# Optimization experiments

Hardware: AMD Instinct MI355X
Metric: run time of the kernel (lower is better)

The kernel has to match this reference:

```python
import jax, jax.numpy as jnp
from jax import lax
import numpy as np

B, CTX, TGT, D_MODEL = 2, 1024, 256, 512
EXPAND, D_STATE, D_CONV, N_LAYERS = 2, 16, 4, 2
D_INNER = EXPAND * D_MODEL
DT_RANK = (D_MODEL + 15) // 16  # 32, mamba_ssm default ceil(d_model/16)
LN_EPS = 1e-5


def setup_inputs() -> dict:
    key = jax.random.key(0)
    ks = jax.random.split(key, 20)
    s = 0.02
    inp = {
        "context_repr": jax.random.normal(ks[0], (B, CTX, D_MODEL), jnp.float32),
        "target_time_emb": jax.random.normal(ks[1], (B, TGT, D_MODEL), jnp.float32),
        "target_var_emb": jax.random.normal(ks[2], (B, TGT, D_MODEL), jnp.float32),
        "target_count": TGT,
        # position_proj / output_proj / LayerNorm params
        "pos_w": jax.random.normal(ks[3], (D_MODEL, 2 * D_MODEL), jnp.float32) * s,
        "pos_b": jnp.zeros((D_MODEL,), jnp.float32),
        "outp_w": jax.random.normal(ks[4], (D_MODEL, D_MODEL), jnp.float32) * s,
        "outp_b": jnp.zeros((D_MODEL,), jnp.float32),
        "ln_g": jnp.ones((D_MODEL,), jnp.float32),
        "ln_b": jnp.zeros((D_MODEL,), jnp.float32),
        # stacked per-layer Mamba params
        "in_w": jax.random.normal(ks[5], (N_LAYERS, 2 * D_INNER, D_MODEL), jnp.float32) * s,
        "conv_w": jax.random.normal(ks[6], (N_LAYERS, D_INNER, D_CONV), jnp.float32) * s,
        "conv_b": jnp.zeros((N_LAYERS, D_INNER), jnp.float32),
        "xproj_w": jax.random.normal(ks[7], (N_LAYERS, DT_RANK + 2 * D_STATE, D_INNER), jnp.float32) * s,
        "dt_w": jax.random.normal(ks[8], (N_LAYERS, D_INNER, DT_RANK), jnp.float32) * s,
        "dt_b": jax.random.normal(ks[9], (N_LAYERS, D_INNER), jnp.float32) * s,
        # A_log init as in mamba_ssm: A = arange(1, d_state+1) repeated over d_inner
        "A_log": jnp.broadcast_to(
            jnp.log(jnp.arange(1, D_STATE + 1, dtype=jnp.float32)),
            (N_LAYERS, D_INNER, D_STATE),
        ).copy(),
        "D_skip": jnp.ones((N_LAYERS, D_INNER), jnp.float32),
        "out_w": jax.random.normal(ks[10], (N_LAYERS, D_MODEL, D_INNER), jnp.float32) * s,
    }
    return inp


def _mamba_block(x, in_w, conv_w, conv_b, xproj_w, dt_w, dt_b, A_log, D_skip, out_w):
    # x: [B, L, d_model]
    Bb, L, _ = x.shape
    xz = jnp.einsum("bld,ed->ble", x, in_w)          # [B, L, 2*d_inner]
    xc, z = jnp.split(xz, 2, axis=-1)
    # causal depthwise conv1d (Conv1d pad=d_conv-1 then [..., :L])
    xt = xc.transpose(0, 2, 1)                        # [B, d_inner, L]
    conv = lax.conv_general_dilated(
        xt, conv_w[:, None, :], (1,), [(D_CONV - 1, 0)],
        feature_group_count=D_INNER,
        dimension_numbers=("NCH", "OIH", "NCH"),
    )
    u = jax.nn.silu(conv + conv_b[None, :, None]).transpose(0, 2, 1)  # [B, L, d_inner]
    x_dbl = jnp.einsum("bld,ed->ble", u, xproj_w)     # [B, L, dt_rank + 2*d_state]
    dt, Bm, Cm = jnp.split(x_dbl, [DT_RANK, DT_RANK + D_STATE], axis=-1)
    delta = jax.nn.softplus(jnp.einsum("blr,dr->bld", dt, dt_w) + dt_b)  # [B, L, d_inner]
    A = -jnp.exp(A_log)                               # [d_inner, d_state]
    dA = jnp.exp(delta[..., None] * A)                # [B, L, d_inner, d_state]
    dBu = delta[..., None] * Bm[:, :, None, :] * u[..., None]

    def step(h, inps):
        dA_t, dBu_t, C_t = inps                       # [B,d_inner,d_state], same, [B,d_state]
        h = dA_t * h + dBu_t
        y = jnp.einsum("bds,bs->bd", h, C_t)
        return h, y

    h0 = jnp.zeros((Bb, D_INNER, D_STATE), x.dtype)
    _, ys = lax.scan(step, h0, (dA.transpose(1, 0, 2, 3), dBu.transpose(1, 0, 2, 3), Cm.transpose(1, 0, 2)))
    y = ys.transpose(1, 0, 2) + u * D_skip            # [B, L, d_inner]
    y = y * jax.nn.silu(z)
    return jnp.einsum("ble,de->bld", y, out_w)        # [B, L, d_model]


def reference(context_repr, target_time_emb, target_var_emb, target_count,
              pos_w, pos_b, outp_w, outp_b, ln_g, ln_b,
              in_w, conv_w, conv_b, xproj_w, dt_w, dt_b, A_log, D_skip, out_w):
    tc = jnp.concatenate([target_time_emb, target_var_emb], axis=-1)      # [B, T, 2*d]
    pos = jnp.einsum("blk,dk->bld", tc, pos_w) + pos_b                    # [B, T, d]
    x = jnp.concatenate([context_repr, pos], axis=1)                      # [B, C+T, d]
    for i in range(N_LAYERS):
        x = x + _mamba_block(x, in_w[i], conv_w[i], conv_b[i], xproj_w[i],
                             dt_w[i], dt_b[i], A_log[i], D_skip[i], out_w[i])
    mu = jnp.mean(x, axis=-1, keepdims=True)
    var = jnp.mean(jnp.square(x - mu), axis=-1, keepdims=True)
    x = (x - mu) * lax.rsqrt(var + LN_EPS) * ln_g + ln_b
    tgt = x[:, -int(target_count):]
    return jnp.einsum("bld,ed->ble", tgt, outp_w) + outp_b
```

## Files before the change

### kernel.cpp

```cpp
#include <hip/hip_runtime.h>
#include <hip/hip_bf16.h>

#define B_     2
#define CTX_   1024
#define TGT_   256
#define DM_    512
#define L_     1280
#define DI_    1024
#define DS_    16
#define DCONV_ 4
#define NL_    2
#define DTR_   32
#define MROWS_ (B_*L_)
#define NC_    80
#define CL_    16
#define XDBL_N_ (MROWS_*64)

typedef unsigned short u16;
typedef __attribute__((ext_vector_type(8))) __bf16 bf16x8;
typedef __attribute__((ext_vector_type(4))) float f32x4;

__device__ __forceinline__ float sigmoidf_(float v){ return 1.f/(1.f+__expf(-v)); }
__device__ __forceinline__ float siluf_(float v){ return v*sigmoidf_(v); }
__device__ __forceinline__ float softplusf_(float v){ return (v>20.f)?v:log1pf(__expf(v)); }
__device__ __forceinline__ u16 f2b(float f){
    union { float f; unsigned u; } x; x.f = f;
    unsigned u = x.u;
    return (u16)((u + 0x7fffu + ((u>>16)&1u)) >> 16);
}
__device__ __forceinline__ float b2f(u16 v){ return __uint_as_float(((unsigned)v)<<16); }
__device__ __forceinline__ void gload_lds16(const void* g, void* l){
    __builtin_amdgcn_global_load_lds((const __attribute__((address_space(1))) unsigned*)g,
                                     (__attribute__((address_space(3))) unsigned*)l, 16, 0, 0);
}
#define PIPE_SYNC do{ asm volatile("s_waitcnt vmcnt(0)" ::: "memory"); \
                      __builtin_amdgcn_sched_barrier(0); \
                      __builtin_amdgcn_s_barrier(); \
                      __builtin_amdgcn_sched_barrier(0); }while(0)

#define G0_ 262144
#define G1_ 131072
#define G2_  65536
#define G3_  32768
#define G4_  16384
__global__ __launch_bounds__(256) void k_init(const float* __restrict__ s0, const float* __restrict__ s1,
                                              const float* __restrict__ s2, const float* __restrict__ s3,
                                              const float* __restrict__ s4,
                                              u16* d0, u16* d1, u16* d2, u16* d3, u16* d4,
                                              const float* __restrict__ ctx, const float* __restrict__ te,
                                              const float* __restrict__ ve, float* __restrict__ x,
                                              u16* __restrict__ xb, u16* __restrict__ tcb){
    int blk = blockIdx.x;
    if (blk < 1984){
        int g = blk*256 + threadIdx.x;
        const float* s; u16* d; int base;
        if      (g < G0_)                { s=s0; d=d0; base=g*8; }
        else if (g < G0_+G1_)            { s=s1; d=d1; base=(g-G0_)*8; }
        else if (g < G0_+G1_+G2_)        { s=s2; d=d2; base=(g-G0_-G1_)*8; }
        else if (g < G0_+G1_+G2_+G3_)    { s=s3; d=d3; base=(g-G0_-G1_-G2_)*8; }
        else                             { s=s4; d=d4; base=(g-G0_-G1_-G2_-G3_)*8; }
        float4 a = *(const float4*)&s[base];
        float4 b = *(const float4*)&s[base+4];
        union { u16 us[8]; uint4 v; } o;
        o.us[0]=f2b(a.x); o.us[1]=f2b(a.y); o.us[2]=f2b(a.z); o.us[3]=f2b(a.w);
        o.us[4]=f2b(b.x); o.us[5]=f2b(b.y); o.us[6]=f2b(b.z); o.us[7]=f2b(b.w);
        *(uint4*)&d[base] = o.v;
    } else if (blk < 1984+1024){
        int e = ((blk-1984)*256 + threadIdx.x)*4;
        int d = e % DM_;
        int l = (e/DM_) % CTX_;
        int b = e/(DM_*CTX_);
        float4 v = *(const float4*)&ctx[e];
        size_t o = ((size_t)(b*L_+l))*DM_ + d;
        *(float4*)&x[o] = v;
        union { u16 us[4]; uint2 q; } p;
        p.us[0]=f2b(v.x); p.us[1]=f2b(v.y); p.us[2]=f2b(v.z); p.us[3]=f2b(v.w);
        *(uint2*)&xb[o] = p.q;
    } else {
        int e = ((blk-1984-1024)*256 + threadIdx.x)*4;
        int k = e % (2*DM_);
        int r = e / (2*DM_);
        float4 v = (k < DM_) ? *(const float4*)&te[(size_t)r*DM_ + k]
                             : *(const float4*)&ve[(size_t)r*DM_ + (k-DM_)];
        union { u16 us[4]; uint2 q; } p;
        p.us[0]=f2b(v.x); p.us[1]=f2b(v.y); p.us[2]=f2b(v.z); p.us[3]=f2b(v.w);
        *(uint2*)&tcb[e] = p.q;
    }
}

template<bool WB>
__global__ __launch_bounds__(512) void k_mmx(const u16* __restrict__ A, int lda,
                                             const u16* __restrict__ Bw, int ldb,
                                             float* __restrict__ C, int ldc,
                                             const float* __restrict__ bias, int K,
                                             u16* __restrict__ Cb, int ldcb){
    __shared__ u16 As[2][128*64];
    __shared__ u16 Bs[2][128*64];
    int tid = threadIdx.x;
    int wave = tid >> 6, lane = tid & 63;
    int bm = blockIdx.y*128, bn = blockIdx.x*128;
    int wr = (wave>>2)*64, wc = (wave&3)*32;
    f32x4 acc[4][2] = {};
    int lrow = lane & 15, lk = (lane>>4)*8;
    int dphys0 = tid*16;
    int dphys1 = dphys0 + 8192;
    int alog0  = dphys0 ^ (((dphys0>>7)&7)<<4);
    int alog1  = dphys1 ^ (((dphys1>>7)&7)<<4);
    int grow0  = alog0 >> 7,         grow1 = alog1 >> 7;
    int gcol0  = (alog0 & 127) >> 1, gcol1 = (alog1 & 127) >> 1;
    const u16* Ar0 = A  + (size_t)(bm+grow0)*lda + gcol0;
    const u16* Ar1 = A  + (size_t)(bm+grow1)*lda + gcol1;
    const u16* Br0 = Bw + (size_t)(bn+grow0)*ldb + gcol0;
    const u16* Br1 = Bw + (size_t)(bn+grow1)*ldb + gcol1;
    int aoff[4][2], boff[2][2];
    #pragma unroll
    for (int f=0; f<4; ++f){
        int ra = wr + f*16 + lrow;
        #pragma unroll
        for (int s=0;s<2;++s) aoff[f][s] = (ra*128 + s*64 + lk*2) ^ ((ra&7)<<4);
    }
    #pragma unroll
    for (int f=0; f<2; ++f){
        int rb = wc + f*16 + lrow;
        #pragma unroll
        for (int s=0;s<2;++s) boff[f][s] = (rb*128 + s*64 + lk*2) ^ ((rb&7)<<4);
    }
    int nt = K >> 6;
    auto stage = [&](int t, int buf){
        int k0 = t*64;
        gload_lds16(Ar0 + k0, &As[buf][wave*512]);
        gload_lds16(Ar1 + k0, &As[buf][4096 + wave*512]);
        gload_lds16(Br0 + k0, &Bs[buf][wave*512]);
        gload_lds16(Br1 + k0, &Bs[buf][4096 + wave*512]);
    };
    stage(0, 0);
    PIPE_SYNC;
    int cur = 0;
    for (int t=0; t<nt; ++t){
        if (t+1 < nt) stage(t+1, cur^1);
        #pragma unroll
        for (int s=0;s<2;++s){
            bf16x8 af[4], bfr[2];
            #pragma unroll
            for (int f=0; f<4; ++f) af[f]  = *(const bf16x8*)((const char*)As[cur] + aoff[f][s]);
            #pragma unroll
            for (int f=0; f<2; ++f) bfr[f] = *(const bf16x8*)((const char*)Bs[cur] + boff[f][s]);
            #pragma unroll
            for (int fm=0; fm<4; ++fm)
                #pragma unroll
                for (int fn=0; fn<2; ++fn)
                    acc[fm][fn] = __builtin_amdgcn_mfma_f32_16x16x32_bf16(af[fm], bfr[fn], acc[fm][fn], 0,0,0);
        }
        PIPE_SYNC;
        cur ^= 1;
    }
    #pragma unroll
    for (int fm=0; fm<4; ++fm){
        int m0 = bm + wr + fm*16 + (lane>>4)*4;
        #pragma unroll
        for (int fn=0; fn<2; ++fn){
            int n = bn + wc + fn*16 + (lane&15);
            float bsv = (!WB && bias) ? bias[n] : 0.f;
            #pragma unroll
            for (int j=0; j<4; ++j){
                float v = acc[fm][fn][j] + bsv;
                if (WB) Cb[(size_t)(m0+j)*ldcb + n] = f2b(v);
                else    C [(size_t)(m0+j)*ldc  + n] = v;
            }
        }
    }
}

template<bool ACC, bool SCAT>
__global__ __launch_bounds__(512) void k_mmx64(const u16* __restrict__ A, int lda,
                                               const u16* __restrict__ Bw, int ldb,
                                               float* __restrict__ C, int ldc,
                                               const float* __restrict__ bias, int ksteps,
                                               u16* __restrict__ Cb, int ldcb){
    __shared__ u16 As[2][64*32];
    __shared__ u16 Bs[2][64*32];
    int tid = threadIdx.x;
    int wave = tid >> 6, lane = tid & 63;
    int bm = blockIdx.y*64;
    int bn = blockIdx.x*64;
    int wr = (wave>>2)*32, wc = (wave&3)*16;
    f32x4 acc[2] = {};
    int lrow = lane & 15, lk = (lane>>4)*8;
    int w4 = wave & 3;
    int dphys = w4*1024 + lane*16;
    int alog  = dphys ^ (((dphys>>7)&7)<<4);
    int grow  = alog >> 6;
    int gcol  = (alog & 63) >> 1;
    bool isB = wave >= 4;
    const u16* Sr = isB ? (Bw + (size_t)(bn+grow)*ldb + gcol)
                        : (A  + (size_t)(bm+grow)*lda + gcol);
    u16* dst0 = isB ? &Bs[0][w4*512] : &As[0][w4*512];
    u16* dst1 = isB ? &Bs[1][w4*512] : &As[1][w4*512];
    int aoff[2], boff;
    #pragma unroll
    for (int f=0; f<2; ++f){
        int ra = wr + f*16 + lrow;
        aoff[f] = (ra*64 + lk*2) ^ (((ra>>1)&7)<<4);
    }
    { int rb = wc + lrow; boff = (rb*64 + lk*2) ^ (((rb>>1)&7)<<4); }
    auto stage = [&](int t, int buf){
        gload_lds16(Sr + t*32, buf ? dst1 : dst0);
    };
    stage(0, 0);
    PIPE_SYNC;
    int cur = 0;
    for (int t = 0; t < ksteps; ++t){
        if (t+1 < ksteps) stage(t+1, cur^1);
        bf16x8 af[2], bfr;
        #pragma unroll
        for (int f=0; f<2; ++f) af[f] = *(const bf16x8*)((const char*)As[cur] + aoff[f]);
        bfr = *(const bf16x8*)((const char*)Bs[cur] + boff);
        #pragma unroll
        for (int fm=0; fm<2; ++fm)
            acc[fm] = __builtin_amdgcn_mfma_f32_16x16x32_bf16(af[fm], bfr, acc[fm], 0,0,0);
        PIPE_SYNC;
        cur ^= 1;
    }
    #pragma unroll
    for (int fm=0; fm<2; ++fm){
        int m0 = bm + wr + fm*16 + (lane>>4)*4;
        int n = bn + wc + (lane&15);
        float bsv = bias ? bias[n] : 0.f;
        #pragma unroll
        for (int j=0; j<4; ++j){
            float v = acc[fm][j] + bsv;
            int m = m0 + j;
            if (SCAT){
                int xrow = (m>>8)*L_ + CTX_ + (m&255);
                C [(size_t)xrow*ldc  + n] = v;
                Cb[(size_t)xrow*ldcb + n] = f2b(v);
            } else {
                size_t off = (size_t)m*ldc + n;
                if (ACC) v += C[off];
                C[off] = v;
                if (Cb) Cb[(size_t)m*ldcb + n] = f2b(v);
            }
        }
    }
}

__global__ __launch_bounds__(512) void k_xproj(const u16* __restrict__ xzb, const u16* __restrict__ Bw,
                                               float* __restrict__ C, const float* __restrict__ cw,
                                               const float* __restrict__ cb){
    __shared__ u16 As[64*32];
    __shared__ u16 Bs[64*32];
    __shared__ u16 sXC[67*32];
    int tid = threadIdx.x;
    int wave = tid >> 6, lane = tid & 63;
    int bm = blockIdx.y*64;
    int kbase = blockIdx.x*128;
    int b0row = (bm/L_)*L_;
    int wr = (wave>>2)*32, wc = (wave&3)*16;
    f32x4 acc[2] = {};
    int lrow = lane & 15, lk = (lane>>4)*8;
    int w4 = wave & 3;
    int dphys = w4*1024 + lane*16;
    int alog  = dphys ^ (((dphys>>7)&7)<<4);
    int grow  = alog >> 6;
    int gcol  = (alog & 63) >> 1;
    const u16* Br = Bw + (size_t)grow*DI_ + gcol;
    int aoff[2], boff;
    #pragma unroll
    for (int f=0; f<2; ++f){
        int ra = wr + f*16 + lrow;
        aoff[f] = (ra*64 + lk*2) ^ (((ra>>1)&7)<<4);
    }
    { int rb = wc + lrow; boff = (rb*64 + lk*2) ^ (((rb>>1)&7)<<4); }
    for (int t = 0; t < 4; ++t){
        int k0 = kbase + t*32;
        if (wave >= 4) gload_lds16(Br + k0, &Bs[w4*512]);
        if (tid < 268){
            int rr = tid >> 2, c16 = (tid & 3)*8;
            int gr = bm + rr - 3;
            uint4 v = make_uint4(0,0,0,0);
            if (gr >= b0row) v = *(const uint4*)&xzb[(size_t)gr*2048 + k0 + c16];
            *(uint4*)&sXC[rr*32 + c16] = v;
        }
        __syncthreads();
        {
            int o = tid*4, rr = o >> 5, cc0 = o & 31;
            union { u16 us[4]; uint2 q; } w;
            #pragma unroll
            for (int j=0;j<4;++j){
                int cc = cc0 + j, d = k0 + cc;
                float4 wv = *(const float4*)&cw[d*4];
                float a = cb[d];
                a = fmaf(b2f(sXC[(rr+0)*32+cc]), wv.x, a);
                a = fmaf(b2f(sXC[(rr+1)*32+cc]), wv.y, a);
                a = fmaf(b2f(sXC[(rr+2)*32+cc]), wv.z, a);
                a = fmaf(b2f(sXC[(rr+3)*32+cc]), wv.w, a);
                w.us[j] = f2b(siluf_(a));
            }
            int L0 = rr*64 + cc0*2;
            int ph = L0 ^ (((L0>>7)&7)<<4);
            *(uint2*)((char*)As + ph) = w.q;
        }
        __syncthreads();
        bf16x8 af[2], bfr;
        #pragma unroll
        for (int f=0; f<2; ++f) af[f] = *(const bf16x8*)((const char*)As + aoff[f]);
        bfr = *(const bf16x8*)((const char*)Bs + boff);
        #pragma unroll
        for (int fm=0; fm<2; ++fm)
            acc[fm] = __builtin_amdgcn_mfma_f32_16x16x32_bf16(af[fm], bfr, acc[fm], 0,0,0);
        __syncthreads();
    }
    float* Cout = C + (size_t)blockIdx.x*XDBL_N_;
    #pragma unroll
    for (int fm=0; fm<2; ++fm){
        int m0 = bm + wr + fm*16 + (lane>>4)*4;
        int n = wc + (lane&15);
        #pragma unroll
        for (int j=0; j<4; ++j)
            Cout[(size_t)(m0+j)*64 + n] = acc[fm][j];
    }
}

__global__ __launch_bounds__(256) void k_red8(const float* __restrict__ part, float* __restrict__ out){
    int j = (blockIdx.x*256 + threadIdx.x)*4;
    float4 s = *(const float4*)&part[j];
    #pragma unroll
    for (int p=1;p<8;++p){
        float4 t = *(const float4*)&part[(size_t)p*XDBL_N_ + j];
        s.x+=t.x; s.y+=t.y; s.z+=t.z; s.w+=t.w;
    }
    *(float4*)&out[j] = s;
}

__global__ __launch_bounds__(256) void k_scan1(const u16* __restrict__ xzb, const float* __restrict__ xdbl,
                                               const float* __restrict__ dtw, const float* __restrict__ dtb,
                                               const float* __restrict__ cw, const float* __restrict__ cb,
                                               const float* __restrict__ Alog,
                                               float* __restrict__ hend, float* __restrict__ P){
    __shared__ float sX[CL_*64];
    __shared__ float sW[64*33];
    __shared__ float sDtb[64];
    __shared__ float sDel[CL_*64];
    __shared__ float sU[CL_*64];
    __shared__ u16   sXC[19*64];
    int blk = blockIdx.x;
    int dgrp = blk & 15;
    int c = (blk>>4) % NC_;
    int b = blk/(16*NC_);
    int d0 = dgrp*64;
    int tid = threadIdx.x;
    size_t rowbase = (size_t)(b*L_ + c*CL_);
    {
        int e = tid*4;
        *(float4*)&sX[e] = *(const float4*)&xdbl[rowbase*64 + e];
        int w0 = tid*8, dr = w0>>5, kk = w0&31;
        float4 wa = *(const float4*)&dtw[(size_t)(d0+dr)*DTR_ + kk];
        float4 wb = *(const float4*)&dtw[(size_t)(d0+dr)*DTR_ + kk + 4];
        sW[dr*33+kk+0]=wa.x; sW[dr*33+kk+1]=wa.y; sW[dr*33+kk+2]=wa.z; sW[dr*33+kk+3]=wa.w;
        sW[dr*33+kk+4]=wb.x; sW[dr*33+kk+5]=wb.y; sW[dr*33+kk+6]=wb.z; sW[dr*33+kk+7]=wb.w;
        if (tid < 64) sDtb[tid] = dtb[d0+tid];
    }
    if (tid < 152){
        int rr = tid >> 3, c8 = (tid & 7)*8;
        long gr = (long)rowbase + rr - 3;
        uint4 v = make_uint4(0,0,0,0);
        if (gr >= (long)b*L_) v = *(const uint4*)&xzb[(size_t)gr*2048 + d0 + c8];
        *(uint4*)&sXC[rr*64 + c8] = v;
    }
    __syncthreads();
    {
        int o = tid*4, t = o>>6, dd0 = o&63;
        #pragma unroll
        for (int j=0;j<4;++j){
            int dd = dd0 + j, d = d0 + dd;
            float4 wv = *(const float4*)&cw[d*4];
            float a = cb[d];
            a = fmaf(b2f(sXC[(t+0)*64+dd]), wv.x, a);
            a = fmaf(b2f(sXC[(t+1)*64+dd]), wv.y, a);
            a = fmaf(b2f(sXC[(t+2)*64+dd]), wv.z, a);
            a = fmaf(b2f(sXC[(t+3)*64+dd]), wv.w, a);
            sU[t*64+dd] = siluf_(a);
        }
    }
    #pragma unroll
    for (int i=0;i<4;++i){
        int idx = tid + i*256;
        int t = idx>>6, dd = idx&63;
        float acc = sDtb[dd];
        #pragma unroll
        for (int k=0;k<DTR_;++k) acc = fmaf(sX[t*64+k], sW[dd*33+k], acc);
        sDel[idx] = softplusf_(acc);
    }
    __syncthreads();
    int dl = tid>>2, sg = (tid&3)*4;
    int d = d0 + dl;
    float A[4];
    #pragma unroll
    for (int i=0;i<4;++i) A[i] = -__expf(Alog[d*DS_ + sg + i]);
    float h[4] = {0,0,0,0}, Pl[4] = {1.f,1.f,1.f,1.f};
    #pragma unroll
    for (int t=0;t<CL_;++t){
        float delta = sDel[t*64+dl];
        float du    = delta*sU[t*64+dl];
        #pragma unroll
        for (int i=0;i<4;++i){
            float a = __expf(delta*A[i]);
            h[i]  = fmaf(a, h[i], du*sX[t*64 + 32 + sg + i]);
            Pl[i] *= a;
        }
    }
    size_t ob = ((size_t)((b*NC_+c)*DI_) + d)*DS_ + sg;
    *(float4*)&hend[ob] = make_float4(h[0],h[1],h[2],h[3]);
    *(float4*)&P[ob]    = make_float4(Pl[0],Pl[1],Pl[2],Pl[3]);
}

__global__ __launch_bounds__(256) void k_scan2(float* __restrict__ hend, const float* __restrict__ P){
    int g = blockIdx.x*256 + threadIdx.x;
    int s = g & 15;
    int d = (g>>4) & 1023;
    int b = g>>14;
    size_t base = ((size_t)b*NC_*DI_ + d)*DS_ + s;
    const size_t cs = (size_t)DI_*DS_;
    float h = 0.f;
    for (int c0=0;c0<NC_;c0+=8){
        float he[8], p[8];
        #pragma unroll
        for (int j=0;j<8;++j){ size_t idx = base + (size_t)(c0+j)*cs; he[j]=hend[idx]; p[j]=P[idx]; }
        #pragma unroll
        for (int j=0;j<8;++j){ size_t idx = base + (size_t)(c0+j)*cs; hend[idx]=h; h=fmaf(p[j],h,he[j]); }
    }
}

__global__ __launch_bounds__(256) void k_scan3(const u16* __restrict__ xzb, const float* __restrict__ xdbl,
                                               const float* __restrict__ dtw, const float* __restrict__ dtb,
                                               const float* __restrict__ cw, const float* __restrict__ cb,
                                               const float* __restrict__ Alog, const float* __restrict__ Dsk,
                                               const float* __restrict__ hstart, u16* __restrict__ yb){
    __shared__ float sX[CL_*64];
    __shared__ float sW[64*33];
    __shared__ float sDtb[64];
    __shared__ float sDel[CL_*64];
    __shared__ float sU[CL_*64];
    __shared__ float sY[CL_*64];
    __shared__ u16   sXC[19*64];
    int blk = blockIdx.x;
    int dgrp = blk & 15;
    int c = (blk>>4) % NC_;
    int b = blk/(16*NC_);
    int d0 = dgrp*64;
    int tid = threadIdx.x;
    size_t rowbase = (size_t)(b*L_ + c*CL_);
    {
        int e = tid*4;
        *(float4*)&sX[e] = *(const float4*)&xdbl[rowbase*64 + e];
        int w0 = tid*8, dr = w0>>5, kk = w0&31;
        float4 wa = *(const float4*)&dtw[(size_t)(d0+dr)*DTR_ + kk];
        float4 wb = *(const float4*)&dtw[(size_t)(d0+dr)*DTR_ + kk + 4];
        sW[dr*33+kk+0]=wa.x; sW[dr*33+kk+1]=wa.y; sW[dr*33+kk+2]=wa.z; sW[dr*33+kk+3]=wa.w;
        sW[dr*33+kk+4]=wb.x; sW[dr*33+kk+5]=wb.y; sW[dr*33+kk+6]=wb.z; sW[dr*33+kk+7]=wb.w;
        if (tid < 64) sDtb[tid] = dtb[d0+tid];
    }
    if (tid < 152){
        int rr = tid >> 3, c8 = (tid & 7)*8;
        long gr = (long)rowbase + rr - 3;
        uint4 v = make_uint4(0,0,0,0);
        if (gr >= (long)b*L_) v = *(const uint4*)&xzb[(size_t)gr*2048 + d0 + c8];
        *(uint4*)&sXC[rr*64 + c8] = v;
    }
    __syncthreads();
    {
        int o = tid*4, t = o>>6, dd0 = o&63;
        #pragma unroll
        for (int j=0;j<4;++j){
            int dd = dd0 + j, d = d0 + dd;
            float4 wv = *(const float4*)&cw[d*4];
            float a = cb[d];
            a = fmaf(b2f(sXC[(t+0)*64+dd]), wv.x, a);
            a = fmaf(b2f(sXC[(t+1)*64+dd]), wv.y, a);
            a = fmaf(b2f(sXC[(t+2)*64+dd]), wv.z, a);
            a = fmaf(b2f(sXC[(t+3)*64+dd]), wv.w, a);
            sU[t*64+dd] = siluf_(a);
        }
    }
    #pragma unroll
    for (int i=0;i<4;++i){
        int idx = tid + i*256;
        int t = idx>>6, dd = idx&63;
        float acc = sDtb[dd];
        #pragma unroll
        for (int k=0;k<DTR_;++k) acc = fmaf(sX[t*64+k], sW[dd*33+k], acc);
        sDel[idx] = softplusf_(acc);
    }
    __syncthreads();
    int dl = tid>>2, sg = (tid&3)*4;
    int d = d0 + dl;
    float A[4];
    #pragma unroll
    for (int i=0;i<4;++i) A[i] = -__expf(Alog[d*DS_ + sg + i]);
    size_t ib = ((size_t)((b*NC_+c)*DI_) + d)*DS_ + sg;
    float4 h4 = *(const float4*)&hstart[ib];
    float h[4] = {h4.x, h4.y, h4.z, h4.w};
    #pragma unroll
    for (int t=0;t<CL_;++t){
        float delta = sDel[t*64+dl];
        float du    = delta*sU[t*64+dl];
        float yt = 0.f;
        #pragma unroll
        for (int i=0;i<4;++i){
            float a = __expf(delta*A[i]);
            h[i] = fmaf(a, h[i], du*sX[t*64 + 32 + sg + i]);
            yt   = fmaf(h[i], sX[t*64 + 48 + sg + i], yt);
        }
        yt += __shfl_xor(yt, 1);
        yt += __shfl_xor(yt, 2);
        if ((tid&3)==0) sY[t*64+dl] = yt;
    }
    __syncthreads();
    {
        int e = tid*4, st = e>>6, dd = e&63;
        size_t off = (rowbase+st)*DI_ + d0 + dd;
        float4 dskv = *(const float4*)&Dsk[d0+dd];
        uint2 zz = *(const uint2*)&xzb[(rowbase+st)*2048 + DI_ + d0 + dd];
        float z0 = __uint_as_float(zz.x<<16),  z1 = __uint_as_float(zz.x & 0xffff0000u);
        float z2 = __uint_as_float(zz.y<<16),  z3 = __uint_as_float(zz.y & 0xffff0000u);
        union { u16 us[4]; uint2 q; } o;
        o.us[0] = f2b((sY[e+0] + sU[e+0]*dskv.x) * siluf_(z0));
        o.us[1] = f2b((sY[e+1] + sU[e+1]*dskv.y) * siluf_(z1));
        o.us[2] = f2b((sY[e+2] + sU[e+2]*dskv.z) * siluf_(z2));
        o.us[3] = f2b((sY[e+3] + sU[e+3]*dskv.w) * siluf_(z3));
        *(uint2*)&yb[off] = o.q;
    }
}

__global__ __launch_bounds__(512) void k_lnmm(const float* __restrict__ x, const float* __restrict__ g_,
                                              const float* __restrict__ be_,
                                              const u16* __restrict__ Bw,
                                              const float* __restrict__ bias, float* __restrict__ out){
    __shared__ u16 ALn[64*512];
    __shared__ u16 Bs[2][64*32];
    int tid = threadIdx.x;
    int wave = tid >> 6, lane = tid & 63;
    int bm = blockIdx.y*64, bn = blockIdx.x*64;
    for (int rr8 = 0; rr8 < 8; ++rr8){
        int rr = wave*8 + rr8;
        int tr = bm + rr;
        int xrow = (tr>>8)*L_ + CTX_ + (tr&255);
        const float* row = x + (size_t)xrow*DM_ + lane*8;
        float4 a = *(const float4*)row;
        float4 b = *(const float4*)(row+4);
        float s  = a.x+a.y+a.z+a.w + b.x+b.y+b.z+b.w;
        float sq = a.x*a.x+a.y*a.y+a.z*a.z+a.w*a.w + b.x*b.x+b.y*b.y+b.z*b.z+b.w*b.w;
        #pragma unroll
        for (int off=32; off; off>>=1){ s += __shfl_xor(s,off); sq += __shfl_xor(sq,off); }
        float mu = s*(1.f/DM_);
        float rs = rsqrtf(sq*(1.f/DM_) - mu*mu + 1e-5f);
        int c0 = lane*8;
        float4 g0 = *(const float4*)&g_[c0],  g1 = *(const float4*)&g_[c0+4];
        float4 b0 = *(const float4*)&be_[c0], b1 = *(const float4*)&be_[c0+4];
        union { u16 us[8]; uint4 v; } o;
        o.us[0]=f2b((a.x-mu)*rs*g0.x+b0.x); o.us[1]=f2b((a.y-mu)*rs*g0.y+b0.y);
        o.us[2]=f2b((a.z-mu)*rs*g0.z+b0.z); o.us[3]=f2b((a.w-mu)*rs*g0.w+b0.w);
        o.us[4]=f2b((b.x-mu)*rs*g1.x+b1.x); o.us[5]=f2b((b.y-mu)*rs*g1.y+b1.y);
        o.us[6]=f2b((b.z-mu)*rs*g1.z+b1.z); o.us[7]=f2b((b.w-mu)*rs*g1.w+b1.w);
        int ph = (rr*1024) + ((lane*16) ^ ((rr&7)<<4));
        *(uint4*)((char*)ALn + ph) = o.v;
    }
    __syncthreads();
    int wr = (wave>>2)*32, wc = (wave&3)*16;
    f32x4 acc[2] = {};
    int lrow = lane & 15, lk = (lane>>4)*8;
    int w4 = wave & 3;
    int dphys = w4*1024 + lane*16;
    int alog  = dphys ^ (((dphys>>7)&7)<<4);
    int grow  = alog >> 6;
    int gcol  = (alog & 63) >> 1;
    const u16* Sr = Bw + (size_t)(bn+grow)*DM_ + gcol;
    int boff;
    { int rb = wc + lrow; boff = (rb*64 + lk*2) ^ (((rb>>1)&7)<<4); }
    int ra0 = wr + lrow, ra1 = wr + 16 + lrow;
    if (wave >= 4) gload_lds16(Sr, &Bs[0][w4*512]);
    PIPE_SYNC;
    int cur = 0;
    for (int t = 0; t < 16; ++t){
        if (t+1 < 16 && wave >= 4) gload_lds16(Sr + (t+1)*32, &Bs[cur^1][w4*512]);
        int kb = (t*32 + lk)*2;
        bf16x8 af0 = *(const bf16x8*)((const char*)ALn + (ra0*1024 + (kb ^ ((ra0&7)<<4))));
        bf16x8 af1 = *(const bf16x8*)((const char*)ALn + (ra1*1024 + (kb ^ ((ra1&7)<<4))));
        bf16x8 bfr = *(const bf16x8*)((const char*)Bs[cur] + boff);
        acc[0] = __builtin_amdgcn_mfma_f32_16x16x32_bf16(af0, bfr, acc[0], 0,0,0);
        acc[1] = __builtin_amdgcn_mfma_f32_16x16x32_bf16(af1, bfr, acc[1], 0,0,0);
        PIPE_SYNC;
        cur ^= 1;
    }
    #pragma unroll
    for (int fm=0; fm<2; ++fm){
        int m0 = bm + wr + fm*16 + (lane>>4)*4;
        int n = bn + wc + (lane&15);
        float bsv = bias[n];
        #pragma unroll
        for (int j=0; j<4; ++j)
            out[(size_t)(m0+j)*DM_ + n] = acc[fm][j] + bsv;
    }
}

extern "C" void kernel_launch(void* const* d_in, const int* in_sizes, int n_in,
                              void* d_out, int out_size, void* d_ws, size_t ws_size,
                              hipStream_t stream) {
    const float* ctx    = (const float*)d_in[0];
    const float* te     = (const float*)d_in[1];
    const float* ve     = (const float*)d_in[2];
    const float* pos_w  = (const float*)d_in[4];
    const float* pos_b  = (const float*)d_in[5];
    const float* outp_w = (const float*)d_in[6];
    const float* outp_b = (const float*)d_in[7];
    const float* ln_g   = (const float*)d_in[8];
    const float* ln_b   = (const float*)d_in[9];
    const float* in_w   = (const float*)d_in[10];
    const float* conv_w = (const float*)d_in[11];
    const float* conv_b = (const float*)d_in[12];
    const float* xproj_w= (const float*)d_in[13];
    const float* dt_w   = (const float*)d_in[14];
    const float* dt_b   = (const float*)d_in[15];
    const float* A_log  = (const float*)d_in[16];
    const float* D_skip = (const float*)d_in[17];
    const float* out_w  = (const float*)d_in[18];
    float* out = (float*)d_out;

    float* ws    = (float*)d_ws;
    float* x     = ws;
    float* hend  = x     + 1310720;
    float* P     = hend  + 2621440;
    float* xdblp = P     + 2621440;
    float* xdbl  = xdblp + 1310720;
    u16*  xb    = (u16*)(xdbl + 163840);
    u16*  tcb   = xb    + 1310720;
    u16*  yb    = tcb   + 524288;
    u16*  xzb   = yb    + 2621440;
    u16*  inwb  = xzb   + 5242880;
    u16*  outwb = inwb  + 2097152;
    u16*  poswb = outwb + 1048576;
    u16*  outpwb= poswb + 524288;
    u16*  xpwb  = outpwb+ 262144;

    k_init<<<3520, 256, 0, stream>>>(in_w, out_w, pos_w, outp_w, xproj_w,
                                     inwb, outwb, poswb, outpwb, xpwb,
                                     ctx, te, ve, x, xb, tcb);
    k_mmx64<false,true><<<dim3(8,8), 512, 0, stream>>>(tcb, 2*DM_, poswb, 2*DM_, x, DM_, pos_b, 32, xb, DM_);

    for (int i=0;i<NL_;++i){
        const u16*   inwbi  = inwb + (size_t)i*2*DI_*DM_;
        const float* cw     = conv_w  + (size_t)i*DI_*DCONV_;
        const float* cb     = conv_b  + (size_t)i*DI_;
        const u16*   xpwbi  = xpwb + (size_t)i*(DTR_+2*DS_)*DI_;
        const float* dtw    = dt_w    + (size_t)i*DI_*DTR_;
        const float* dtb    = dt_b    + (size_t)i*DI_;
        const float* Ai     = A_log   + (size_t)i*DI_*DS_;
        const float* Dsk    = D_skip  + (size_t)i*DI_;
        const u16*   outwbi = outwb + (size_t)i*DM_*DI_;

        k_mmx<true><<<dim3(16,20), 512, 0, stream>>>(xb, DM_, inwbi, DM_, nullptr, 0, nullptr, DM_, xzb, 2*DI_);
        k_xproj<<<dim3(8,40), 512, 0, stream>>>(xzb, xpwbi, xdblp, cw, cb);
        k_red8<<<160, 256, 0, stream>>>(xdblp, xdbl);
        k_scan1<<<2560, 256, 0, stream>>>(xzb, xdbl, dtw, dtb, cw, cb, Ai, hend, P);
        k_scan2<<<128, 256, 0, stream>>>(hend, P);
        k_scan3<<<2560, 256, 0, stream>>>(xzb, xdbl, dtw, dtb, cw, cb, Ai, Dsk, hend, yb);
        k_mmx64<true,false><<<dim3(8,40), 512, 0, stream>>>(yb, DI_, outwbi, DI_, x, DM_, nullptr, 32, xb, DM_);
    }

    k_lnmm<<<dim3(8,8), 512, 0, stream>>>(x, ln_g, ln_b, outpwb, outp_b, out);
}
```

Measured before the change: 224.8 us.

## Double scan chunk length and add XCD-aware block swizzle to GEMMs

Halves the number of scan chunks (80→40) while doubling chunk length (16→32), adjusting the scan kernels' loads, LDS halo buffers and grid sizes, and shrinking the chunk-state workspace. This cuts the per-chunk overhead of reloading weights and conv halos and the carry-propagation work, at the cost of longer sequential recurrences per block and half as many blocks. It also remaps workgroup IDs in the GEMM kernels so consecutive tiles land on the same XCD, aiming for better L2 reuse.

Result: slower. 231.7 us (+3.1%).

```diff
diff --git a/kernel.cpp b/kernel.cpp
--- a/kernel.cpp
+++ b/kernel.cpp
@@ -12,8 +12,8 @@
 #define NL_    2
 #define DTR_   32
 #define MROWS_ (B_*L_)
-#define NC_    80
-#define CL_    16
+#define NC_    40
+#define CL_    32
 #define XDBL_N_ (MROWS_*64)
 
 typedef unsigned short u16;
@@ -37,6 +37,12 @@
                       __builtin_amdgcn_sched_barrier(0); \
                       __builtin_amdgcn_s_barrier(); \
                       __builtin_amdgcn_sched_barrier(0); }while(0)
+
+#define XCD_SWZ(bx, by) \
+    int nwg_ = gridDim.x*gridDim.y; \
+    int id_  = blockIdx.y*gridDim.x + blockIdx.x; \
+    int swz_ = (id_ & 7)*(nwg_>>3) + (id_>>3); \
+    int bx = swz_ % gridDim.x, by = swz_ / gridDim.x;
 
 #define G0_ 262144
 #define G1_ 131072
@@ -98,7 +104,8 @@
     __shared__ u16 Bs[2][128*64];
     int tid = threadIdx.x;
     int wave = tid >> 6, lane = tid & 63;
-    int bm = blockIdx.y*128, bn = blockIdx.x*128;
+    XCD_SWZ(bx, by);
+    int bm = by*128, bn = bx*128;
     int wr = (wave>>2)*64, wc = (wave&3)*32;
     f32x4 acc[4][2] = {};
     int lrow = lane & 15, lk = (lane>>4)*8;
@@ -181,8 +188,9 @@
     __shared__ u16 Bs[2][64*32];
     int tid = threadIdx.x;
     int wave = tid >> 6, lane = tid & 63;
-    int bm = blockIdx.y*64;
-    int bn = blockIdx.x*64;
+    XCD_SWZ(bx, by);
+    int bm = by*64;
+    int bn = bx*64;
     int wr = (wave>>2)*32, wc = (wave&3)*16;
     f32x4 acc[2] = {};
     int lrow = lane & 15, lk = (lane>>4)*8;
@@ -252,8 +260,9 @@
     __shared__ u16 sXC[67*32];
     int tid = threadIdx.x;
     int wave = tid >> 6, lane = tid & 63;
-    int bm = blockIdx.y*64;
-    int kbase = blockIdx.x*128;
+    XCD_SWZ(bx, by);
+    int bm = by*64;
+    int kbase = bx*128;
     int b0row = (bm/L_)*L_;
     int wr = (wave>>2)*32, wc = (wave&3)*16;
     f32x4 acc[2] = {};
@@ -310,7 +319,7 @@
             acc[fm] = __builtin_amdgcn_mfma_f32_16x16x32_bf16(af[fm], bfr, acc[fm], 0,0,0);
         __syncthreads();
     }
-    float* Cout = C + (size_t)blockIdx.x*XDBL_N_;
+    float* Cout = C + (size_t)bx*XDBL_N_;
     #pragma unroll
     for (int fm=0; fm<2; ++fm){
         int m0 = bm + wr + fm*16 + (lane>>4)*4;
@@ -342,7 +351,7 @@
     __shared__ float sDtb[64];
     __shared__ float sDel[CL_*64];
     __shared__ float sU[CL_*64];
-    __shared__ u16   sXC[19*64];
+    __shared__ u16   sXC[35*64];
     int blk = blockIdx.x;
     int dgrp = blk & 15;
     int c = (blk>>4) % NC_;
@@ -350,9 +359,12 @@
     int d0 = dgrp*64;
     int tid = threadIdx.x;
     size_t rowbase = (size_t)(b*L_ + c*CL_);
+    #pragma unroll
+    for (int j=0;j<2;++j){
+        int e = tid*4 + j*1024;
+        *(float4*)&sX[e] = *(const float4*)&xdbl[rowbase*64 + e];
+    }
     {
-        int e = tid*4;
-        *(float4*)&sX[e] = *(const float4*)&xdbl[rowbase*64 + e];
         int w0 = tid*8, dr = w0>>5, kk = w0&31;
         float4 wa = *(const float4*)&dtw[(size_t)(d0+dr)*DTR_ + kk];
         float4 wb = *(const float4*)&dtw[(size_t)(d0+dr)*DTR_ + kk + 4];
@@ -360,19 +372,20 @@
         sW[dr*33+kk+4]=wb.x; sW[dr*33+kk+5]=wb.y; sW[dr*33+kk+6]=wb.z; sW[dr*33+kk+7]=wb.w;
         if (tid < 64) sDtb[tid] = dtb[d0+tid];
     }
-    if (tid < 152){
-        int rr = tid >> 3, c8 = (tid & 7)*8;
+    for (int i = tid; i < 280; i += 256){
+        int rr = i >> 3, c8 = (i & 7)*8;
         long gr = (long)rowbase + rr - 3;
         uint4 v = make_uint4(0,0,0,0);
         if (gr >= (long)b*L_) v = *(const uint4*)&xzb[(size_t)gr*2048 + d0 + c8];
         *(uint4*)&sXC[rr*64 + c8] = v;
     }
     __syncthreads();
-    {
-        int o = tid*4, t = o>>6, dd0 = o&63;
-        #pragma unroll
-        for (int j=0;j<4;++j){
-            int dd = dd0 + j, d = d0 + dd;
+    #pragma unroll
+    for (int j=0;j<2;++j){
+        int o = tid*4 + j*1024, t = o>>6, dd0 = o&63;
+        #pragma unroll
+        for (int jj=0;jj<4;++jj){
+            int dd = dd0 + jj, d = d0 + dd;
             float4 wv = *(const float4*)&cw[d*4];
             float a = cb[d];
             a = fmaf(b2f(sXC[(t+0)*64+dd]), wv.x, a);
@@ -383,7 +396,7 @@
         }
     }
     #pragma unroll
-    for (int i=0;i<4;++i){
+    for (int i=0;i<8;++i){
         int idx = tid + i*256;
         int t = idx>>6, dd = idx&63;
         float acc = sDtb[dd];
@@ -442,7 +455,7 @@
     __shared__ float sDel[CL_*64];
     __shared__ float sU[CL_*64];
     __shared__ float sY[CL_*64];
-    __shared__ u16   sXC[19*64];
+    __shared__ u16   sXC[35*64];
     int blk = blockIdx.x;
     int dgrp = blk & 15;
     int c = (blk>>4) % NC_;
@@ -450,9 +463,12 @@
     int d0 = dgrp*64;
     int tid = threadIdx.x;
     size_t rowbase = (size_t)(b*L_ + c*CL_);
+    #pragma unroll
+    for (int j=0;j<2;++j){
+        int e = tid*4 + j*1024;
+        *(float4*)&sX[e] = *(const float4*)&xdbl[rowbase*64 + e];
+    }
     {
-        int e = tid*4;
-        *(float4*)&sX[e] = *(const float4*)&xdbl[rowbase*64 + e];
         int w0 = tid*8, dr = w0>>5, kk = w0&31;
         float4 wa = *(const float4*)&dtw[(size_t)(d0+dr)*DTR_ + kk];
         float4 wb = *(const float4*)&dtw[(size_t)(d0+dr)*DTR_ + kk + 4];
@@ -460,19 +476,20 @@
         sW[dr*33+kk+4]=wb.x; sW[dr*33+kk+5]=wb.y; sW[dr*33+kk+6]=wb.z; sW[dr*33+kk+7]=wb.w;
         if (tid < 64) sDtb[tid] = dtb[d0+tid];
     }
-    if (tid < 152){
-        int rr = tid >> 3, c8 = (tid & 7)*8;
+    for (int i = tid; i < 280; i += 256){
+        int rr = i >> 3, c8 = (i & 7)*8;
         long gr = (long)rowbase + rr - 3;
         uint4 v = make_uint4(0,0,0,0);
         if (gr >= (long)b*L_) v = *(const uint4*)&xzb[(size_t)gr*2048 + d0 + c8];
         *(uint4*)&sXC[rr*64 + c8] = v;
     }
     __syncthreads();
-    {
-        int o = tid*4, t = o>>6, dd0 = o&63;
-        #pragma unroll
-        for (int j=0;j<4;++j){
-            int dd = dd0 + j, d = d0 + dd;
+    #pragma unroll
+    for (int j=0;j<2;++j){
+        int o = tid*4 + j*1024, t = o>>6, dd0 = o&63;
+        #pragma unroll
+        for (int jj=0;jj<4;++jj){
+            int dd = dd0 + jj, d = d0 + dd;
             float4 wv = *(const float4*)&cw[d*4];
             float a = cb[d];
             a = fmaf(b2f(sXC[(t+0)*64+dd]), wv.x, a);
@@ -483,7 +500,7 @@
         }
     }
     #pragma unroll
-    for (int i=0;i<4;++i){
+    for (int i=0;i<8;++i){
         int idx = tid + i*256;
         int t = idx>>6, dd = idx&63;
         float acc = sDtb[dd];
@@ -516,8 +533,9 @@
         if ((tid&3)==0) sY[t*64+dl] = yt;
     }
     __syncthreads();
-    {
-        int e = tid*4, st = e>>6, dd = e&63;
+    #pragma unroll
+    for (int j=0;j<2;++j){
+        int e = tid*4 + j*1024, st = e>>6, dd = e&63;
         size_t off = (rowbase+st)*DI_ + d0 + dd;
         float4 dskv = *(const float4*)&Dsk[d0+dd];
         uint2 zz = *(const uint2*)&xzb[(rowbase+st)*2048 + DI_ + d0 + dd];
@@ -629,8 +647,8 @@
     float* ws    = (float*)d_ws;
     float* x     = ws;
     float* hend  = x     + 1310720;
-    float* P     = hend  + 2621440;
-    float* xdblp = P     + 2621440;
+    float* P     = hend  + 1310720;
+    float* xdblp = P     + 1310720;
     float* xdbl  = xdblp + 1310720;
     u16*  xb    = (u16*)(xdbl + 163840);
     u16*  tcb   = xb    + 1310720;
@@ -661,9 +679,9 @@
         k_mmx<true><<<dim3(16,20), 512, 0, stream>>>(xb, DM_, inwbi, DM_, nullptr, 0, nullptr, DM_, xzb, 2*DI_);
         k_xproj<<<dim3(8,40), 512, 0, stream>>>(xzb, xpwbi, xdblp, cw, cb);
         k_red8<<<160, 256, 0, stream>>>(xdblp, xdbl);
-        k_scan1<<<2560, 256, 0, stream>>>(xzb, xdbl, dtw, dtb, cw, cb, Ai, hend, P);
+        k_scan1<<<1280, 256, 0, stream>>>(xzb, xdbl, dtw, dtb, cw, cb, Ai, hend, P);
         k_scan2<<<128, 256, 0, stream>>>(hend, P);
-        k_scan3<<<2560, 256, 0, stream>>>(xzb, xdbl, dtw, dtb, cw, cb, Ai, Dsk, hend, yb);
+        k_scan3<<<1280, 256, 0, stream>>>(xzb, xdbl, dtw, dtb, cw, cb, Ai, Dsk, hend, yb);
         k_mmx64<true,false><<<dim3(8,40), 512, 0, stream>>>(yb, DI_, outwbi, DI_, x, DM_, nullptr, 32, xb, DM_);
     }
 
```
